# Kernel optimization log

Measured on AMD Instinct MI355X. Metric: run time of the kernel, lower is better.

The kernel has to match this reference:

```python
import jax, jax.numpy as jnp
from jax import lax
import numpy as np

B, V, T, P, F, H = 128, 24, 30, 15, 4, 256


def setup_inputs() -> dict:
    key = jax.random.key(0)
    ks = jax.random.split(key, 12)
    w = lambda k, shape: (jax.random.normal(k, shape, jnp.float32) * 0.05)
    return {
        "sequence": jax.random.normal(ks[0], (B, V, T, F), jnp.float32),
        "dist_matrix": jax.random.normal(ks[1], (B, V, T, V), jnp.float32),
        "bearing_matrix": jax.random.normal(ks[2], (B, V, T, V), jnp.float32),
        "heading_matrix": jax.random.normal(ks[3], (B, V, T, V), jnp.float32),
        "seq_mask": jnp.ones((B, V, T), bool),
        "op_mask": jnp.ones((B, V), bool),
        "W_ih_enc": w(ks[4], (4 * H, F)),
        "W_hh_enc": w(ks[5], (4 * H, H)),
        "b_ih_enc": jnp.zeros((4 * H,), jnp.float32),
        "b_hh_enc": jnp.zeros((4 * H,), jnp.float32),
        "W_ih_dec": w(ks[6], (4 * H, F)),
        "W_hh_dec": w(ks[7], (4 * H, H)),
        "b_ih_dec": jnp.zeros((4 * H,), jnp.float32),
        "b_hh_dec": jnp.zeros((4 * H,), jnp.float32),
        "W_out": w(ks[8], (F, H)),
        "b_out": jnp.zeros((F,), jnp.float32),
    }


def lstm_cell(x, h, c, Wih, Whh, bih, bhh):
    # torch LSTMCell gate order: i, f, g, o
    gates = x @ Wih.T + h @ Whh.T + (bih + bhh)
    i, f, g, o = jnp.split(gates, 4, axis=-1)
    c_new = jax.nn.sigmoid(f) * c + jax.nn.sigmoid(i) * jnp.tanh(g)
    h_new = jax.nn.sigmoid(o) * jnp.tanh(c_new)
    return h_new, c_new


def reference(sequence, dist_matrix, bearing_matrix, heading_matrix, seq_mask, op_mask,
              W_ih_enc, W_hh_enc, b_ih_enc, b_hh_enc,
              W_ih_dec, W_hh_dec, b_ih_dec, b_hh_dec,
              W_out, b_out):
    Bn, Vn, Tn, Fn = sequence.shape
    Hn = W_hh_enc.shape[1]
    h0 = jnp.zeros((Bn, Vn, Hn), sequence.dtype)
    c0 = jnp.zeros((Bn, Vn, Hn), sequence.dtype)

    # ---- encoder: batched over vessels, scanned over time ----
    def enc_step(carry, inp):
        h, c = carry
        x_t, m_t = inp  # [B,V,F], [B,V]
        h, c = lstm_cell(x_t, h, c, W_ih_enc, W_hh_enc, b_ih_enc, b_hh_enc)
        h = jnp.where(m_t[..., None], h, 0.0)  # masked_fill of hidden
        return (h, c), h

    xs = (sequence.transpose(2, 0, 1, 3), seq_mask.transpose(2, 0, 1))
    (h, c), enc_hs = lax.scan(enc_step, (h0, c0), xs)
    encoded = enc_hs.transpose(1, 2, 0, 3)  # [B,V,T,H]

    opm = seq_mask[:, :, -1]  # [B,V] (op_mask used in decode)

    # ---- decoder: temporal attention + LSTMCell, scanned over prediction steps ----
    def dec_step(carry, _):
        h, c, prev = carry
        scores = jnp.einsum('bvth,bvh->bvt', encoded, h)
        scores = jnp.where(seq_mask, scores, -1e9)
        alpha = jax.nn.softmax(scores, axis=-1)  # alignment vector [B,V,T]
        ctx = jnp.einsum('bvt,bvth->bvh', alpha, encoded)  # attended hidden
        h2, c2 = lstm_cell(prev, ctx, c, W_ih_dec, W_hh_dec, b_ih_dec, b_hh_dec)
        h2 = jnp.where(opm[..., None], h2, 0.0)
        pred = jax.nn.relu(h2 @ W_out.T + b_out)  # [B,V,F]
        pred = jnp.where(opm[..., None], pred, 0.0)
        return (h2, c2, pred), (pred, alpha)
    prev0 = sequence[:, :, -1, :]
    _, (preds, aligns) = lax.scan(dec_step, (h, c, prev0), None, length=P)
    output = preds.transpose(1, 2, 0, 3)   # [B,V,P,F]
    alignments = aligns                    # [P,B,V,T]
    return output, alignments
```

## Files before the change

### kernel.cpp

```cpp
#include <hip/hip_runtime.h>
#include <hip/hip_bf16.h>

#define TDIM 30
#define PDIM 15
#define FDIM 4
#define HDIM 256
#define NROWS 3072
#define NBLK 192
#define SEQ_STRIDE (TDIM * FDIM)

using bf16x8 = __attribute__((ext_vector_type(8))) __bf16;
using f32x4  = __attribute__((ext_vector_type(4))) float;

__device__ __forceinline__ float sigf(float x) {
    return 1.0f / (1.0f + __expf(-x));
}
__device__ __forceinline__ float tanh_fast(float x) {
    const float e = __expf(2.0f * x);
    return 1.0f - 2.0f / (e + 1.0f);
}
__device__ __forceinline__ float bf16_hi(unsigned int u) { return __uint_as_float(u << 16); }
__device__ __forceinline__ float bf16_lo(unsigned int u) { return __uint_as_float(u & 0xffff0000u); }

__global__ __launch_bounds__(256) void prep_kernel(
    const float* __restrict__ Whh_e, const float* __restrict__ Whh_d,
    const float* __restrict__ bih_e, const float* __restrict__ bhh_e,
    const float* __restrict__ bih_d, const float* __restrict__ bhh_d,
    __hip_bfloat16* __restrict__ Wfe, __hip_bfloat16* __restrict__ Wfd,
    float* __restrict__ bsum_e, float* __restrict__ bsum_d)
{
    const int b = blockIdx.x, tid = threadIdx.x;
    if (b < 256) {
        const int m = b >> 7;
        const int id = (b & 127) * 256 + tid;
        const int frag = id >> 6, lane = id & 63;
        const int ks = frag & 7, q = (frag >> 3) & 3, cj = frag >> 5;
        const int gcol = q * 256 + cj * 16 + (lane & 15);
        const int k0 = ks * 32 + (lane >> 4) * 8;
        const float* W = m ? Whh_d : Whh_e;
        __hip_bfloat16* Wf = m ? Wfd : Wfe;
        const float* src = W + (size_t)gcol * HDIM + k0;
        __hip_bfloat16* dst = Wf + (size_t)frag * 512 + lane * 8;
#pragma unroll
        for (int e = 0; e < 8; ++e) dst[e] = __float2bfloat16(src[e]);
    } else {
        const int id = (b - 256) * 256 + tid;
        if (id < 1024) bsum_e[id] = bih_e[id] + bhh_e[id];
        else if (id < 2048) { const int k = id - 1024; bsum_d[k] = bih_d[k] + bhh_d[k]; }
    }
}

__global__ __launch_bounds__(512, 2) void persistent_kernel(
    const float* __restrict__ seq,
    const __hip_bfloat16* __restrict__ Wfe, const __hip_bfloat16* __restrict__ Wfd,
    const float* __restrict__ Wih_e, const float* __restrict__ bsum_e,
    const float* __restrict__ Wih_d, const float* __restrict__ bsum_d,
    const float* __restrict__ Wout, const float* __restrict__ bout,
    __hip_bfloat16* __restrict__ enc,
    float* __restrict__ out, float* __restrict__ align_base)
{
    __shared__ __hip_bfloat16 h_hi[16][264];
    __shared__ __hip_bfloat16 h_lo[16][264];
    __shared__ __hip_bfloat16 ctx_lds[16][264];
    __shared__ float s_buf[16][32];
    __shared__ float prev_lds[16][4];

    const int tid = threadIdx.x;
    const int w = tid >> 6, lane = tid & 63;
    const int lrow = lane & 15, lk = lane >> 4;
    const int R0 = blockIdx.x * 16;

    for (int i = tid; i < 16 * 264; i += 512) {
        (&h_hi[0][0])[i] = __float2bfloat16(0.0f);
        (&h_lo[0][0])[i] = __float2bfloat16(0.0f);
    }
    if (tid < 64)
        prev_lds[tid >> 2][tid & 3] =
            seq[(size_t)(R0 + (tid >> 2)) * SEQ_STRIDE + (TDIM - 1) * FDIM + (tid & 3)];
    float c[2][4] = {{0.f,0.f,0.f,0.f},{0.f,0.f,0.f,0.f}};
    __syncthreads();

    for (int t = 0; t < TDIM; ++t) {
        bf16x8 ahi[8], alo[8];
#pragma unroll
        for (int ks = 0; ks < 8; ++ks) {
            ahi[ks] = *reinterpret_cast<const bf16x8*>(&h_hi[lrow][ks * 32 + lk * 8]);
            alo[ks] = *reinterpret_cast<const bf16x8*>(&h_lo[lrow][ks * 32 + lk * 8]);
        }
        float4 xr[4];
#pragma unroll
        for (int r = 0; r < 4; ++r)
            xr[r] = *reinterpret_cast<const float4*>(
                &seq[(size_t)(R0 + lk * 4 + r) * SEQ_STRIDE + t * FDIM]);
        __syncthreads();

#pragma unroll
        for (int j = 0; j < 2; ++j) {
            const int col = w * 32 + j * 16 + lrow;
            const __hip_bfloat16* wb = Wfe + ((size_t)(w * 2 + j) * 32) * 512 + lane * 8;
            f32x4 acc[4];
#pragma unroll
            for (int q = 0; q < 4; ++q) acc[q] = (f32x4){0.f,0.f,0.f,0.f};
#pragma unroll
            for (int q = 0; q < 4; ++q) {
#pragma unroll
                for (int ks = 0; ks < 8; ++ks) {
                    const bf16x8 bfr = *reinterpret_cast<const bf16x8*>(wb + (q * 8 + ks) * 512);
                    acc[q] = __builtin_amdgcn_mfma_f32_16x16x32_bf16(alo[ks], bfr, acc[q], 0, 0, 0);
                    acc[q] = __builtin_amdgcn_mfma_f32_16x16x32_bf16(ahi[ks], bfr, acc[q], 0, 0, 0);
                }
            }
            float bs[4]; float4 wih[4];
#pragma unroll
            for (int q = 0; q < 4; ++q) {
                bs[q] = bsum_e[q * 256 + col];
                wih[q] = *reinterpret_cast<const float4*>(&Wih_e[(size_t)(q * 256 + col) * FDIM]);
            }
#pragma unroll
            for (int r = 0; r < 4; ++r) {
                const int row = lk * 4 + r;
                float g[4];
#pragma unroll
                for (int q = 0; q < 4; ++q)
                    g[q] = acc[q][r] + bs[q] + xr[r].x * wih[q].x + xr[r].y * wih[q].y
                         + xr[r].z * wih[q].z + xr[r].w * wih[q].w;
                const float ig = sigf(g[0]), fg = sigf(g[1]);
                const float gg = tanh_fast(g[2]), og = sigf(g[3]);
                const float cn = fg * c[j][r] + ig * gg;
                c[j][r] = cn;
                const float hn = og * tanh_fast(cn);
                const __hip_bfloat16 hhi = __float2bfloat16(hn);
                h_hi[row][col] = hhi;
                h_lo[row][col] = __float2bfloat16(hn - __bfloat162float(hhi));
                enc[((size_t)(R0 + row) * TDIM + t) * HDIM + col] = hhi;
            }
        }
        __syncthreads();
    }

    const int arow = tid >> 5, kt = tid & 31;
    for (int p = 0; p < PDIM; ++p) {
        float hreg[8];
        {
            const uint4 uh = *reinterpret_cast<const uint4*>(&h_hi[arow][kt * 8]);
            const uint4 ul = *reinterpret_cast<const uint4*>(&h_lo[arow][kt * 8]);
            hreg[0] = bf16_hi(uh.x) + bf16_hi(ul.x); hreg[1] = bf16_lo(uh.x) + bf16_lo(ul.x);
            hreg[2] = bf16_hi(uh.y) + bf16_hi(ul.y); hreg[3] = bf16_lo(uh.y) + bf16_lo(ul.y);
            hreg[4] = bf16_hi(uh.z) + bf16_hi(ul.z); hreg[5] = bf16_lo(uh.z) + bf16_lo(ul.z);
            hreg[6] = bf16_hi(uh.w) + bf16_hi(ul.w); hreg[7] = bf16_lo(uh.w) + bf16_lo(ul.w);
        }
        float m = -3.0e38f, l = 0.0f, cacc[8];
#pragma unroll
        for (int i = 0; i < 8; ++i) cacc[i] = 0.0f;
        const __hip_bfloat16* ebase = enc + ((size_t)(R0 + arow) * TDIM) * HDIM + kt * 8;
        for (int tt = 0; tt < TDIM; ++tt) {
            const uint4 ue = *reinterpret_cast<const uint4*>(ebase + tt * HDIM);
            float ev[8];
            ev[0] = bf16_hi(ue.x); ev[1] = bf16_lo(ue.x);
            ev[2] = bf16_hi(ue.y); ev[3] = bf16_lo(ue.y);
            ev[4] = bf16_hi(ue.z); ev[5] = bf16_lo(ue.z);
            ev[6] = bf16_hi(ue.w); ev[7] = bf16_lo(ue.w);
            float s = 0.0f;
#pragma unroll
            for (int i = 0; i < 8; ++i) s += ev[i] * hreg[i];
#pragma unroll
            for (int off = 16; off; off >>= 1) s += __shfl_xor(s, off);
            if (kt == 0) s_buf[arow][tt] = s;
            const float mn = fmaxf(m, s);
            const float scale = __expf(m - mn);
            const float e = __expf(s - mn);
            l = l * scale + e;
            m = mn;
#pragma unroll
            for (int i = 0; i < 8; ++i) cacc[i] = cacc[i] * scale + e * ev[i];
        }
        const float invl = 1.0f / l;
#pragma unroll
        for (int i = 0; i < 8; ++i)
            ctx_lds[arow][kt * 8 + i] = __float2bfloat16(cacc[i] * invl);
        if (kt < TDIM)
            align_base[(size_t)p * NROWS * TDIM + (size_t)(R0 + arow) * TDIM + kt] =
                __expf(s_buf[arow][kt] - m) * invl;
        __syncthreads();

        bf16x8 actx[8];
#pragma unroll
        for (int ks = 0; ks < 8; ++ks)
            actx[ks] = *reinterpret_cast<const bf16x8*>(&ctx_lds[lrow][ks * 32 + lk * 8]);
        float4 xr[4];
#pragma unroll
        for (int r = 0; r < 4; ++r)
            xr[r] = *reinterpret_cast<const float4*>(&prev_lds[lk * 4 + r][0]);

#pragma unroll
        for (int j = 0; j < 2; ++j) {
            const int col = w * 32 + j * 16 + lrow;
            const __hip_bfloat16* wb = Wfd + ((size_t)(w * 2 + j) * 32) * 512 + lane * 8;
            f32x4 acc[4];
#pragma unroll
            for (int q = 0; q < 4; ++q) acc[q] = (f32x4){0.f,0.f,0.f,0.f};
#pragma unroll
            for (int q = 0; q < 4; ++q) {
#pragma unroll
                for (int ks = 0; ks < 8; ++ks) {
                    const bf16x8 bfr = *reinterpret_cast<const bf16x8*>(wb + (q * 8 + ks) * 512);
                    acc[q] = __builtin_amdgcn_mfma_f32_16x16x32_bf16(actx[ks], bfr, acc[q], 0, 0, 0);
                }
            }
            float bs[4]; float4 wih[4];
#pragma unroll
            for (int q = 0; q < 4; ++q) {
                bs[q] = bsum_d[q * 256 + col];
                wih[q] = *reinterpret_cast<const float4*>(&Wih_d[(size_t)(q * 256 + col) * FDIM]);
            }
#pragma unroll
            for (int r = 0; r < 4; ++r) {
                const int row = lk * 4 + r;
                float g[4];
#pragma unroll
                for (int q = 0; q < 4; ++q)
                    g[q] = acc[q][r] + bs[q] + xr[r].x * wih[q].x + xr[r].y * wih[q].y
                         + xr[r].z * wih[q].z + xr[r].w * wih[q].w;
                const float ig = sigf(g[0]), fg = sigf(g[1]);
                const float gg = tanh_fast(g[2]), og = sigf(g[3]);
                const float cn = fg * c[j][r] + ig * gg;
                c[j][r] = cn;
                const float hn = og * tanh_fast(cn);
                const __hip_bfloat16 hhi = __float2bfloat16(hn);
                h_hi[row][col] = hhi;
                h_lo[row][col] = __float2bfloat16(hn - __bfloat162float(hhi));
            }
        }
        __syncthreads();

        {
            const int oid = tid >> 3, sub = tid & 7;
            const int row = oid >> 2, f = oid & 3;
            float s = 0.0f;
#pragma unroll
            for (int kk = 0; kk < 32; kk += 4) {
                const int k = sub * 32 + kk;
                const float4 wv = *reinterpret_cast<const float4*>(&Wout[(size_t)f * HDIM + k]);
                s += (__bfloat162float(h_hi[row][k+0]) + __bfloat162float(h_lo[row][k+0])) * wv.x
                   + (__bfloat162float(h_hi[row][k+1]) + __bfloat162float(h_lo[row][k+1])) * wv.y
                   + (__bfloat162float(h_hi[row][k+2]) + __bfloat162float(h_lo[row][k+2])) * wv.z
                   + (__bfloat162float(h_hi[row][k+3]) + __bfloat162float(h_lo[row][k+3])) * wv.w;
            }
#pragma unroll
            for (int off = 4; off; off >>= 1) s += __shfl_xor(s, off);
            if (sub == 0) {
                const float v = fmaxf(s + bout[f], 0.0f);
                out[(size_t)(R0 + row) * PDIM * FDIM + p * FDIM + f] = v;
                prev_lds[row][f] = v;
            }
        }
        __syncthreads();
    }
}

extern "C" void kernel_launch(void* const* d_in, const int* in_sizes, int n_in,
                              void* d_out, int out_size, void* d_ws, size_t ws_size,
                              hipStream_t stream) {
    const float* seq   = (const float*)d_in[0];
    const float* Wih_e = (const float*)d_in[6];
    const float* Whh_e = (const float*)d_in[7];
    const float* bih_e = (const float*)d_in[8];
    const float* bhh_e = (const float*)d_in[9];
    const float* Wih_d = (const float*)d_in[10];
    const float* Whh_d = (const float*)d_in[11];
    const float* bih_d = (const float*)d_in[12];
    const float* bhh_d = (const float*)d_in[13];
    const float* Wout  = (const float*)d_in[14];
    const float* bout  = (const float*)d_in[15];

    float* out = (float*)d_out;
    float* align_base = out + NROWS * PDIM * FDIM;

    char* wsp = (char*)d_ws;
    __hip_bfloat16* Wfe = (__hip_bfloat16*)wsp; wsp += (size_t)4 * HDIM * HDIM * 2;
    __hip_bfloat16* Wfd = (__hip_bfloat16*)wsp; wsp += (size_t)4 * HDIM * HDIM * 2;
    float* bsum_e = (float*)wsp; wsp += 1024 * 4;
    float* bsum_d = (float*)wsp; wsp += 1024 * 4;
    __hip_bfloat16* enc = (__hip_bfloat16*)wsp; wsp += (size_t)NROWS * TDIM * HDIM * 2;

    prep_kernel<<<264, 256, 0, stream>>>(
        Whh_e, Whh_d, bih_e, bhh_e, bih_d, bhh_d, Wfe, Wfd, bsum_e, bsum_d);

    persistent_kernel<<<NBLK, 512, 0, stream>>>(
        seq, Wfe, Wfd, Wih_e, bsum_e, Wih_d, bsum_d, Wout, bout,
        enc, out, align_base);
}
```

Baseline: 859.6 us.

## Spread LSTM rows over 256 blocks of 1024 threads, one column tile per wave

Each block now handles 12 rows instead of 16, giving 256 blocks so every CU on the device gets work. Blocks are 1024 threads with each wave owning a single 16-column tile instead of two. Weight fragments are double-buffered in registers, and the per-column bias and input weights are hoisted out of the time loop. Attention is reworked to one wave per row, and the padded rows 12-15 waste a quarter of the MFMA work while fewer waves per CU may hurt latency hiding.

```diff
diff --git a/kernel.cpp b/kernel.cpp
--- a/kernel.cpp
+++ b/kernel.cpp
@@ -6,7 +6,8 @@
 #define FDIM 4
 #define HDIM 256
 #define NROWS 3072
-#define NBLK 192
+#define RPB 12
+#define NBLK (NROWS / RPB)
 #define SEQ_STRIDE (TDIM * FDIM)
 
 using bf16x8 = __attribute__((ext_vector_type(8))) __bf16;
@@ -50,7 +51,7 @@
     }
 }
 
-__global__ __launch_bounds__(512, 2) void persistent_kernel(
+__global__ __launch_bounds__(1024, 1) void persistent_kernel(
     const float* __restrict__ seq,
     const __hip_bfloat16* __restrict__ Wfe, const __hip_bfloat16* __restrict__ Wfd,
     const float* __restrict__ Wih_e, const float* __restrict__ bsum_e,
@@ -62,23 +63,37 @@
     __shared__ __hip_bfloat16 h_hi[16][264];
     __shared__ __hip_bfloat16 h_lo[16][264];
     __shared__ __hip_bfloat16 ctx_lds[16][264];
-    __shared__ float s_buf[16][32];
     __shared__ float prev_lds[16][4];
 
     const int tid = threadIdx.x;
     const int w = tid >> 6, lane = tid & 63;
     const int lrow = lane & 15, lk = lane >> 4;
-    const int R0 = blockIdx.x * 16;
-
-    for (int i = tid; i < 16 * 264; i += 512) {
+    const int R0 = blockIdx.x * RPB;
+    const int cj = w;
+    const int col = cj * 16 + lrow;
+
+    for (int i = tid; i < 16 * 264; i += 1024) {
         (&h_hi[0][0])[i] = __float2bfloat16(0.0f);
         (&h_lo[0][0])[i] = __float2bfloat16(0.0f);
-    }
-    if (tid < 64)
-        prev_lds[tid >> 2][tid & 3] =
-            seq[(size_t)(R0 + (tid >> 2)) * SEQ_STRIDE + (TDIM - 1) * FDIM + (tid & 3)];
-    float c[2][4] = {{0.f,0.f,0.f,0.f},{0.f,0.f,0.f,0.f}};
+        (&ctx_lds[0][0])[i] = __float2bfloat16(0.0f);
+    }
+    if (tid < 64) {
+        const int r = tid >> 2, f = tid & 3;
+        prev_lds[r][f] = (r < RPB)
+            ? seq[(size_t)(R0 + r) * SEQ_STRIDE + (TDIM - 1) * FDIM + f] : 0.0f;
+    }
+    float c[4] = {0.f, 0.f, 0.f, 0.f};
     __syncthreads();
+
+    const __hip_bfloat16* wbe = Wfe + (size_t)cj * 32 * 512 + (size_t)lane * 8;
+    const __hip_bfloat16* wbd = Wfd + (size_t)cj * 32 * 512 + (size_t)lane * 8;
+
+    float bs[4]; float4 wih[4];
+#pragma unroll
+    for (int q = 0; q < 4; ++q) {
+        bs[q] = bsum_e[q * 256 + col];
+        wih[q] = *reinterpret_cast<const float4*>(&Wih_e[(size_t)(q * 256 + col) * FDIM]);
+    }
 
     for (int t = 0; t < TDIM; ++t) {
         bf16x8 ahi[8], alo[8];
@@ -89,33 +104,39 @@
         }
         float4 xr[4];
 #pragma unroll
-        for (int r = 0; r < 4; ++r)
-            xr[r] = *reinterpret_cast<const float4*>(
-                &seq[(size_t)(R0 + lk * 4 + r) * SEQ_STRIDE + t * FDIM]);
-        __syncthreads();
-
-#pragma unroll
-        for (int j = 0; j < 2; ++j) {
-            const int col = w * 32 + j * 16 + lrow;
-            const __hip_bfloat16* wb = Wfe + ((size_t)(w * 2 + j) * 32) * 512 + lane * 8;
-            f32x4 acc[4];
-#pragma unroll
-            for (int q = 0; q < 4; ++q) acc[q] = (f32x4){0.f,0.f,0.f,0.f};
-#pragma unroll
-            for (int q = 0; q < 4; ++q) {
-#pragma unroll
-                for (int ks = 0; ks < 8; ++ks) {
-                    const bf16x8 bfr = *reinterpret_cast<const bf16x8*>(wb + (q * 8 + ks) * 512);
-                    acc[q] = __builtin_amdgcn_mfma_f32_16x16x32_bf16(alo[ks], bfr, acc[q], 0, 0, 0);
-                    acc[q] = __builtin_amdgcn_mfma_f32_16x16x32_bf16(ahi[ks], bfr, acc[q], 0, 0, 0);
+        for (int r = 0; r < 4; ++r) {
+            int gr = R0 + lk * 4 + r; if (gr >= NROWS) gr = NROWS - 1;
+            xr[r] = *reinterpret_cast<const float4*>(&seq[(size_t)gr * SEQ_STRIDE + t * FDIM]);
+        }
+        __syncthreads();
+
+        f32x4 acc[4];
+        bf16x8 b0[8], b1[8];
+#pragma unroll
+        for (int ks = 0; ks < 8; ++ks) b0[ks] = *reinterpret_cast<const bf16x8*>(wbe + ks * 512);
+#pragma unroll
+        for (int q = 0; q < 4; ++q) {
+            acc[q] = (f32x4){0.f, 0.f, 0.f, 0.f};
+            if (q < 3) {
+                if ((q & 1) == 0) {
+#pragma unroll
+                    for (int ks = 0; ks < 8; ++ks)
+                        b1[ks] = *reinterpret_cast<const bf16x8*>(wbe + ((q + 1) * 8 + ks) * 512);
+                } else {
+#pragma unroll
+                    for (int ks = 0; ks < 8; ++ks)
+                        b0[ks] = *reinterpret_cast<const bf16x8*>(wbe + ((q + 1) * 8 + ks) * 512);
                 }
             }
-            float bs[4]; float4 wih[4];
-#pragma unroll
-            for (int q = 0; q < 4; ++q) {
-                bs[q] = bsum_e[q * 256 + col];
-                wih[q] = *reinterpret_cast<const float4*>(&Wih_e[(size_t)(q * 256 + col) * FDIM]);
-            }
+#pragma unroll
+            for (int ks = 0; ks < 8; ++ks) {
+                const bf16x8 bfr = ((q & 1) == 0) ? b0[ks] : b1[ks];
+                acc[q] = __builtin_amdgcn_mfma_f32_16x16x32_bf16(alo[ks], bfr, acc[q], 0, 0, 0);
+                acc[q] = __builtin_amdgcn_mfma_f32_16x16x32_bf16(ahi[ks], bfr, acc[q], 0, 0, 0);
+            }
+        }
+
+        if (lk < 3) {
 #pragma unroll
             for (int r = 0; r < 4; ++r) {
                 const int row = lk * 4 + r;
@@ -126,8 +147,8 @@
                          + xr[r].z * wih[q].z + xr[r].w * wih[q].w;
                 const float ig = sigf(g[0]), fg = sigf(g[1]);
                 const float gg = tanh_fast(g[2]), og = sigf(g[3]);
-                const float cn = fg * c[j][r] + ig * gg;
-                c[j][r] = cn;
+                const float cn = fg * c[r] + ig * gg;
+                c[r] = cn;
                 const float hn = og * tanh_fast(cn);
                 const __hip_bfloat16 hhi = __float2bfloat16(hn);
                 h_hi[row][col] = hhi;
@@ -138,49 +159,49 @@
         __syncthreads();
     }
 
-    const int arow = tid >> 5, kt = tid & 31;
+#pragma unroll
+    for (int q = 0; q < 4; ++q) {
+        bs[q] = bsum_d[q * 256 + col];
+        wih[q] = *reinterpret_cast<const float4*>(&Wih_d[(size_t)(q * 256 + col) * FDIM]);
+    }
+
+    const int arow = w;
     for (int p = 0; p < PDIM; ++p) {
-        float hreg[8];
-        {
-            const uint4 uh = *reinterpret_cast<const uint4*>(&h_hi[arow][kt * 8]);
-            const uint4 ul = *reinterpret_cast<const uint4*>(&h_lo[arow][kt * 8]);
-            hreg[0] = bf16_hi(uh.x) + bf16_hi(ul.x); hreg[1] = bf16_lo(uh.x) + bf16_lo(ul.x);
-            hreg[2] = bf16_hi(uh.y) + bf16_hi(ul.y); hreg[3] = bf16_lo(uh.y) + bf16_lo(ul.y);
-            hreg[4] = bf16_hi(uh.z) + bf16_hi(ul.z); hreg[5] = bf16_lo(uh.z) + bf16_lo(ul.z);
-            hreg[6] = bf16_hi(uh.w) + bf16_hi(ul.w); hreg[7] = bf16_lo(uh.w) + bf16_lo(ul.w);
-        }
-        float m = -3.0e38f, l = 0.0f, cacc[8];
-#pragma unroll
-        for (int i = 0; i < 8; ++i) cacc[i] = 0.0f;
-        const __hip_bfloat16* ebase = enc + ((size_t)(R0 + arow) * TDIM) * HDIM + kt * 8;
-        for (int tt = 0; tt < TDIM; ++tt) {
-            const uint4 ue = *reinterpret_cast<const uint4*>(ebase + tt * HDIM);
-            float ev[8];
-            ev[0] = bf16_hi(ue.x); ev[1] = bf16_lo(ue.x);
-            ev[2] = bf16_hi(ue.y); ev[3] = bf16_lo(ue.y);
-            ev[4] = bf16_hi(ue.z); ev[5] = bf16_lo(ue.z);
-            ev[6] = bf16_hi(ue.w); ev[7] = bf16_lo(ue.w);
-            float s = 0.0f;
-#pragma unroll
-            for (int i = 0; i < 8; ++i) s += ev[i] * hreg[i];
-#pragma unroll
-            for (int off = 16; off; off >>= 1) s += __shfl_xor(s, off);
-            if (kt == 0) s_buf[arow][tt] = s;
-            const float mn = fmaxf(m, s);
-            const float scale = __expf(m - mn);
-            const float e = __expf(s - mn);
-            l = l * scale + e;
-            m = mn;
-#pragma unroll
-            for (int i = 0; i < 8; ++i) cacc[i] = cacc[i] * scale + e * ev[i];
-        }
-        const float invl = 1.0f / l;
-#pragma unroll
-        for (int i = 0; i < 8; ++i)
-            ctx_lds[arow][kt * 8 + i] = __float2bfloat16(cacc[i] * invl);
-        if (kt < TDIM)
-            align_base[(size_t)p * NROWS * TDIM + (size_t)(R0 + arow) * TDIM + kt] =
-                __expf(s_buf[arow][kt] - m) * invl;
+        if (arow < RPB) {
+            float hreg[4];
+            {
+                const uint2 uh = *reinterpret_cast<const uint2*>(&h_hi[arow][lane * 4]);
+                const uint2 ul = *reinterpret_cast<const uint2*>(&h_lo[arow][lane * 4]);
+                hreg[0] = bf16_hi(uh.x) + bf16_hi(ul.x); hreg[1] = bf16_lo(uh.x) + bf16_lo(ul.x);
+                hreg[2] = bf16_hi(uh.y) + bf16_hi(ul.y); hreg[3] = bf16_lo(uh.y) + bf16_lo(ul.y);
+            }
+            float m = -3.0e38f, l = 0.0f, s_keep = 0.0f, cacc[4] = {0.f, 0.f, 0.f, 0.f};
+            const __hip_bfloat16* ebase = enc + ((size_t)(R0 + arow) * TDIM) * HDIM + lane * 4;
+            for (int tt = 0; tt < TDIM; ++tt) {
+                const uint2 ue = *reinterpret_cast<const uint2*>(ebase + tt * HDIM);
+                float ev[4];
+                ev[0] = bf16_hi(ue.x); ev[1] = bf16_lo(ue.x);
+                ev[2] = bf16_hi(ue.y); ev[3] = bf16_lo(ue.y);
+                float s = ev[0] * hreg[0] + ev[1] * hreg[1] + ev[2] * hreg[2] + ev[3] * hreg[3];
+#pragma unroll
+                for (int off = 32; off; off >>= 1) s += __shfl_xor(s, off);
+                if (tt == lane) s_keep = s;
+                const float mn = fmaxf(m, s);
+                const float scale = __expf(m - mn);
+                const float e = __expf(s - mn);
+                l = l * scale + e;
+                m = mn;
+#pragma unroll
+                for (int i = 0; i < 4; ++i) cacc[i] = cacc[i] * scale + e * ev[i];
+            }
+            const float invl = 1.0f / l;
+#pragma unroll
+            for (int i = 0; i < 4; ++i)
+                ctx_lds[arow][lane * 4 + i] = __float2bfloat16(cacc[i] * invl);
+            if (lane < TDIM)
+                align_base[(size_t)p * NROWS * TDIM + (size_t)(R0 + arow) * TDIM + lane] =
+                    __expf(s_keep - m) * invl;
+        }
         __syncthreads();
 
         bf16x8 actx[8];
@@ -192,27 +213,32 @@
         for (int r = 0; r < 4; ++r)
             xr[r] = *reinterpret_cast<const float4*>(&prev_lds[lk * 4 + r][0]);
 
-#pragma unroll
-        for (int j = 0; j < 2; ++j) {
-            const int col = w * 32 + j * 16 + lrow;
-            const __hip_bfloat16* wb = Wfd + ((size_t)(w * 2 + j) * 32) * 512 + lane * 8;
-            f32x4 acc[4];
-#pragma unroll
-            for (int q = 0; q < 4; ++q) acc[q] = (f32x4){0.f,0.f,0.f,0.f};
-#pragma unroll
-            for (int q = 0; q < 4; ++q) {
-#pragma unroll
-                for (int ks = 0; ks < 8; ++ks) {
-                    const bf16x8 bfr = *reinterpret_cast<const bf16x8*>(wb + (q * 8 + ks) * 512);
-                    acc[q] = __builtin_amdgcn_mfma_f32_16x16x32_bf16(actx[ks], bfr, acc[q], 0, 0, 0);
+        f32x4 acc[4];
+        bf16x8 b0[8], b1[8];
+#pragma unroll
+        for (int ks = 0; ks < 8; ++ks) b0[ks] = *reinterpret_cast<const bf16x8*>(wbd + ks * 512);
+#pragma unroll
+        for (int q = 0; q < 4; ++q) {
+            acc[q] = (f32x4){0.f, 0.f, 0.f, 0.f};
+            if (q < 3) {
+                if ((q & 1) == 0) {
+#pragma unroll
+                    for (int ks = 0; ks < 8; ++ks)
+                        b1[ks] = *reinterpret_cast<const bf16x8*>(wbd + ((q + 1) * 8 + ks) * 512);
+                } else {
+#pragma unroll
+                    for (int ks = 0; ks < 8; ++ks)
+                        b0[ks] = *reinterpret_cast<const bf16x8*>(wbd + ((q + 1) * 8 + ks) * 512);
                 }
             }
-            float bs[4]; float4 wih[4];
-#pragma unroll
-            for (int q = 0; q < 4; ++q) {
-                bs[q] = bsum_d[q * 256 + col];
-                wih[q] = *reinterpret_cast<const float4*>(&Wih_d[(size_t)(q * 256 + col) * FDIM]);
-            }
+#pragma unroll
+            for (int ks = 0; ks < 8; ++ks) {
+                const bf16x8 bfr = ((q & 1) == 0) ? b0[ks] : b1[ks];
+                acc[q] = __builtin_amdgcn_mfma_f32_16x16x32_bf16(actx[ks], bfr, acc[q], 0, 0, 0);
+            }
+        }
+
+        if (lk < 3) {
 #pragma unroll
             for (int r = 0; r < 4; ++r) {
                 const int row = lk * 4 + r;
@@ -223,8 +249,8 @@
                          + xr[r].z * wih[q].z + xr[r].w * wih[q].w;
                 const float ig = sigf(g[0]), fg = sigf(g[1]);
                 const float gg = tanh_fast(g[2]), og = sigf(g[3]);
-                const float cn = fg * c[j][r] + ig * gg;
-                c[j][r] = cn;
+                const float cn = fg * c[r] + ig * gg;
+                c[r] = cn;
                 const float hn = og * tanh_fast(cn);
                 const __hip_bfloat16 hhi = __float2bfloat16(hn);
                 h_hi[row][col] = hhi;
@@ -234,24 +260,27 @@
         __syncthreads();
 
         {
-            const int oid = tid >> 3, sub = tid & 7;
-            const int row = oid >> 2, f = oid & 3;
-            float s = 0.0f;
-#pragma unroll
-            for (int kk = 0; kk < 32; kk += 4) {
-                const int k = sub * 32 + kk;
-                const float4 wv = *reinterpret_cast<const float4*>(&Wout[(size_t)f * HDIM + k]);
-                s += (__bfloat162float(h_hi[row][k+0]) + __bfloat162float(h_lo[row][k+0])) * wv.x
-                   + (__bfloat162float(h_hi[row][k+1]) + __bfloat162float(h_lo[row][k+1])) * wv.y
-                   + (__bfloat162float(h_hi[row][k+2]) + __bfloat162float(h_lo[row][k+2])) * wv.z
-                   + (__bfloat162float(h_hi[row][k+3]) + __bfloat162float(h_lo[row][k+3])) * wv.w;
-            }
-#pragma unroll
-            for (int off = 4; off; off >>= 1) s += __shfl_xor(s, off);
-            if (sub == 0) {
-                const float v = fmaxf(s + bout[f], 0.0f);
-                out[(size_t)(R0 + row) * PDIM * FDIM + p * FDIM + f] = v;
-                prev_lds[row][f] = v;
+            const int oid = tid >> 4, sub = tid & 15;
+            if (oid < RPB * FDIM) {
+                const int row = oid >> 2, f = oid & 3;
+                float s = 0.0f;
+                const int k0 = sub * 16;
+#pragma unroll
+                for (int kk = 0; kk < 16; kk += 4) {
+                    const int k = k0 + kk;
+                    const float4 wv = *reinterpret_cast<const float4*>(&Wout[(size_t)f * HDIM + k]);
+                    s += (__bfloat162float(h_hi[row][k+0]) + __bfloat162float(h_lo[row][k+0])) * wv.x
+                       + (__bfloat162float(h_hi[row][k+1]) + __bfloat162float(h_lo[row][k+1])) * wv.y
+                       + (__bfloat162float(h_hi[row][k+2]) + __bfloat162float(h_lo[row][k+2])) * wv.z
+                       + (__bfloat162float(h_hi[row][k+3]) + __bfloat162float(h_lo[row][k+3])) * wv.w;
+                }
+#pragma unroll
+                for (int off = 8; off; off >>= 1) s += __shfl_xor(s, off);
+                if (sub == 0) {
+                    const float v = fmaxf(s + bout[f], 0.0f);
+                    out[(size_t)(R0 + row) * PDIM * FDIM + p * FDIM + f] = v;
+                    prev_lds[row][f] = v;
+                }
             }
         }
         __syncthreads();
@@ -286,7 +315,7 @@
     prep_kernel<<<264, 256, 0, stream>>>(
         Whh_e, Whh_d, bih_e, bhh_e, bih_d, bhh_d, Wfe, Wfd, bsum_e, bsum_d);
 
-    persistent_kernel<<<NBLK, 512, 0, stream>>>(
+    persistent_kernel<<<NBLK, 1024, 0, stream>>>(
         seq, Wfe, Wfd, Wih_e, bsum_e, Wih_d, bsum_d, Wout, bout,
         enc, out, align_base);
 }
```

New measurement: 893.9 us. +4.0%, slower.
